# Performance work log

Hardware: AMD Instinct MI355X
Metric: run time of the kernel (lower is better)

Reference implementation:

```python
import jax, jax.numpy as jnp
import numpy as np

N_NODES = 100000
N_EDGES = 1600000
N_GRAPHS = 64
IN_DIM = 256
OUT_DIM = 512
H1 = OUT_DIM // 4   # 128
H2 = OUT_DIM // 2   # 256


def glorot(key, shape):
    lim = float(np.sqrt(6.0 / (shape[0] + shape[1])))
    return jax.random.uniform(key, shape, jnp.float32, -lim, lim)


def setup_inputs() -> dict:
    key = jax.random.key(0)
    ks = jax.random.split(key, 8)
    x = jax.random.normal(ks[0], (N_NODES, IN_DIM), jnp.float32)
    edge_index = jax.random.randint(ks[1], (2, N_EDGES), 0, N_NODES, jnp.int64)
    batch = jnp.sort(jax.random.randint(ks[2], (N_NODES,), 0, N_GRAPHS, jnp.int64))
    return {
        'x': x,
        'edge_index': edge_index,
        'batch': batch,
        'W1': glorot(ks[3], (IN_DIM, H1)),
        'b1': jnp.zeros((H1,), jnp.float32),
        'W2': glorot(ks[4], (H1, H2)),
        'b2': jnp.zeros((H2,), jnp.float32),
        'fc_W': glorot(ks[5], (H2, OUT_DIM)),
        'fc_b': jnp.zeros((OUT_DIM,), jnp.float32),
    }


def gcn_conv(x, W, b, src, dst, n_nodes):
    # PyG GCNConv (default): add self-loops, sym-normalized aggregation of XW + bias
    h = x @ W                                   # [N, F_out] transform first (cheaper gather)
    ones = jnp.ones((src.shape[0],), h.dtype)
    deg = jax.ops.segment_sum(ones, dst, num_segments=n_nodes)  # includes self-loops
    dinv = jax.lax.rsqrt(jnp.maximum(deg, 1.0))
    norm = dinv[src] * dinv[dst]                # [E]
    msg = h[src] * norm[:, None]                # gather + scale
    out = jax.ops.segment_sum(msg, dst, num_segments=n_nodes)   # scatter-add
    return out + b


def reference(x, edge_index, batch, W1, b1, W2, b2, fc_W, fc_b):
    n = x.shape[0]
    loops = jnp.arange(n, dtype=edge_index.dtype)
    src = jnp.concatenate([edge_index[0], loops])
    dst = jnp.concatenate([edge_index[1], loops])

    h = jax.nn.relu(gcn_conv(x, W1, b1, src, dst, n))   # dropout = identity (eval)
    h = jax.nn.relu(gcn_conv(h, W2, b2, src, dst, n))

    # global_mean_pool over batch ids
    sums = jax.ops.segment_sum(h, batch, num_segments=N_GRAPHS)
    cnts = jax.ops.segment_sum(jnp.ones((n,), h.dtype), batch, num_segments=N_GRAPHS)
    pooled = sums / jnp.maximum(cnts, 1.0)[:, None]     # [B, H2]

    return jax.nn.relu(pooled @ fc_W + fc_b)            # [B, OUT_DIM]
```

## Files before the change

### kernel.cpp

```cpp
#include <hip/hip_runtime.h>
#include <hip/hip_bf16.h>
#include <cstdint>

#define N_NODES 100000
#define N_EDGES 1600000
#define N_GRAPHS 64
#define IN_DIM 256
#define HD1 128
#define HD2 256
#define OUT_DIM 512

#define NBUCK 196
#define NBLK  196
#define EPB   8192

typedef __bf16 bf16x8 __attribute__((ext_vector_type(8)));
typedef float f32x4 __attribute__((ext_vector_type(4)));

static __device__ __forceinline__ float bflo(uint32_t v) { return __uint_as_float(v << 16); }
static __device__ __forceinline__ float bfhi(uint32_t v) { return __uint_as_float(v & 0xffff0000u); }
static __device__ __forceinline__ uint32_t f2bf_bits(float f) {
    uint32_t u = __float_as_uint(f);
    return (u + 0x7fffu + ((u >> 16) & 1u)) >> 16;
}
static __device__ __forceinline__ uint32_t packbf(float a, float b) {
    return f2bf_bits(a) | (f2bf_bits(b) << 16);
}
static __device__ __forceinline__ float bf2f(uint16_t b) { return __uint_as_float(((uint32_t)b) << 16); }

static __device__ __forceinline__ void gl_lds16(const void* g, void* l) {
    __builtin_amdgcn_global_load_lds((const __attribute__((address_space(1))) uint32_t*)g,
                                     (__attribute__((address_space(3))) uint32_t*)l, 16, 0, 0);
}

__global__ void k_probe(const uint32_t* __restrict__ xw, const int* __restrict__ ei,
                        int* __restrict__ flags) {
    if (threadIdx.x != 0 || blockIdx.x != 0) return;
    int mid = 0;
    for (int i = 0; i < 64; i++) {
        uint32_t f = (xw[i] >> 23) & 0xFF;
        if (f >= 64 && f < 200) mid++;
    }
    flags[0] = (mid < 32) ? 1 : 0;
    int nz = 0;
    for (int i = 0; i < 64; i++) if (ei[2 * i + 1] != 0) nz++;
    flags[1] = (nz == 0) ? 1 : 0;
}

static __device__ __forceinline__ int ld_idx(const int* p, int i, int sh) { return p[i << sh]; }
static __device__ __forceinline__ float ld_f(const void* p, int i, int isbf) {
    return isbf ? bf2f(((const uint16_t*)p)[i]) : ((const float*)p)[i];
}

__global__ __launch_bounds__(256) void k_prep(const void* __restrict__ W1, const void* __restrict__ W2,
                                              const void* __restrict__ fcW, const void* __restrict__ b1,
                                              const void* __restrict__ b2, const void* __restrict__ fcb,
                                              uint16_t* __restrict__ W1F, uint16_t* __restrict__ W2F,
                                              uint16_t* __restrict__ fcWc, uint16_t* __restrict__ bc1,
                                              uint16_t* __restrict__ bc2, uint16_t* __restrict__ fcbc,
                                              const int* __restrict__ flags) {
    int i = blockIdx.x * 256 + threadIdx.x;
    int isbf = flags[0];
    if (i < 32768) {
        int j = i & 7, l = (i >> 3) & 63, nt = (i >> 9) & 1, ks = (i >> 10) & 7, n0g = (i >> 13) & 3;
        int k = ks * 32 + (l >> 4) * 8 + j;
        int n = n0g * 32 + nt * 16 + (l & 15);
        W1F[i] = (uint16_t)f2bf_bits(ld_f(W1, k * HD1 + n, isbf));
    } else if (i < 65536) {
        int j2 = i - 32768;
        int j = j2 & 7, l = (j2 >> 3) & 63, nt = (j2 >> 9) & 1, ks = (j2 >> 10) & 3, n0g = (j2 >> 12) & 7;
        int k = ks * 32 + (l >> 4) * 8 + j;
        int n = n0g * 32 + nt * 16 + (l & 15);
        W2F[j2] = (uint16_t)f2bf_bits(ld_f(W2, k * HD2 + n, isbf));
    } else if (i < 196608) {
        int j = i - 65536;
        fcWc[j] = (uint16_t)f2bf_bits(ld_f(fcW, j, isbf));
    } else if (i < 196736) {
        bc1[i - 196608] = (uint16_t)f2bf_bits(ld_f(b1, i - 196608, isbf));
    } else if (i < 196992) {
        bc2[i - 196736] = (uint16_t)f2bf_bits(ld_f(b2, i - 196736, isbf));
    } else if (i < 197504) {
        fcbc[i - 196992] = (uint16_t)f2bf_bits(ld_f(fcb, i - 196992, isbf));
    }
}


__global__ __launch_bounds__(256) void k_hist(const int* __restrict__ ei, int* __restrict__ bh,
                                              const int* __restrict__ flags) {
    __shared__ int h[NBUCK];
    int t = threadIdx.x, blk = blockIdx.x;
    if (t < NBUCK) h[t] = 0;
    __syncthreads();
    int sh = flags[1];
    int base = blk * EPB;
#pragma unroll
    for (int k = 0; k < EPB / 256; k++) {
        int e = base + k * 256 + t;
        if (e < N_EDGES) atomicAdd(&h[ld_idx(ei, N_EDGES + e, sh) >> 9], 1);
    }
    __syncthreads();
    if (t < NBUCK) bh[blk * NBUCK + t] = h[t];
}

__global__ __launch_bounds__(256) void k_colscan(const int* __restrict__ bh, int* __restrict__ bhoff,
                                                 int* __restrict__ bucket_cnt) {
    __shared__ int s[256];
    int b = blockIdx.x, t = threadIdx.x;
    int v = (t < NBLK) ? bh[t * NBUCK + b] : 0;
    s[t] = v; __syncthreads();
    for (int off = 1; off < 256; off <<= 1) {
        int x = (t >= off) ? s[t - off] : 0;
        __syncthreads();
        s[t] += x;
        __syncthreads();
    }
    if (t < NBLK) bhoff[t * NBUCK + b] = s[t] - v;
    if (t == 255) bucket_cnt[b] = s[255];
}

__global__ __launch_bounds__(256) void k_bscan(const int* __restrict__ bucket_cnt,
                                               int* __restrict__ bucket_base,
                                               int* __restrict__ row_ptr) {
    __shared__ int s[256];
    int t = threadIdx.x;
    int v = (t < NBUCK) ? bucket_cnt[t] : 0;
    s[t] = v; __syncthreads();
    for (int off = 1; off < 256; off <<= 1) {
        int x = (t >= off) ? s[t - off] : 0;
        __syncthreads();
        s[t] += x;
        __syncthreads();
    }
    if (t < NBUCK) bucket_base[t] = s[t] - v;
    if (t == NBUCK - 1) { bucket_base[NBUCK] = s[t]; row_ptr[N_NODES] = s[t]; }
}

__global__ __launch_bounds__(256) void k_part(const int* __restrict__ ei,
                                              const int* __restrict__ bucket_base,
                                              const int* __restrict__ bhoff,
                                              int* __restrict__ tmp,
                                              const int* __restrict__ flags) {
    __shared__ int cur[NBUCK];
    int t = threadIdx.x, blk = blockIdx.x;
    if (t < NBUCK) cur[t] = bucket_base[t] + bhoff[blk * NBUCK + t];
    __syncthreads();
    int sh = flags[1];
    int base = blk * EPB;
#pragma unroll
    for (int k = 0; k < EPB / 256; k++) {
        int e = base + k * 256 + t;
        if (e < N_EDGES) {
            int s = ld_idx(ei, e, sh), d = ld_idx(ei, N_EDGES + e, sh);
            int pos = atomicAdd(&cur[d >> 9], 1);
            tmp[pos] = (s << 9) | (d & 511);
        }
    }
}

__global__ __launch_bounds__(256) void k_bsort(const int* __restrict__ tmp,
                                               const int* __restrict__ bucket_base,
                                               int* __restrict__ csr_src,
                                               int* __restrict__ row_ptr,
                                               float* __restrict__ dinv) {
    __shared__ int h[512], a[512], c[512];
    int b = blockIdx.x, t = threadIdx.x;
    int beg = bucket_base[b], end = bucket_base[b + 1];
    h[t] = 0; h[t + 256] = 0;
    __syncthreads();
    for (int i = beg + t; i < end; i += 256) atomicAdd(&h[tmp[i] & 511], 1);
    __syncthreads();
    a[t] = h[t]; a[t + 256] = h[t + 256];
    __syncthreads();
    for (int off = 1; off < 512; off <<= 1) {
        int x0 = (t >= off) ? a[t - off] : 0;
        int x1 = ((t + 256) >= off) ? a[t + 256 - off] : 0;
        __syncthreads();
        a[t] += x0; a[t + 256] += x1;
        __syncthreads();
    }
#pragma unroll
    for (int u = 0; u < 2; u++) {
        int i = t + u * 256;
        int node = (b << 9) + i;
        int ex = a[i] - h[i];
        if (node < N_NODES) {
            row_ptr[node] = beg + ex;
            dinv[node] = rsqrtf((float)(h[i] + 1));
        }
        c[i] = ex;
    }
    __syncthreads();
    for (int i = beg + t; i < end; i += 256) {
        int e = tmp[i];
        int pos = atomicAdd(&c[e & 511], 1);
        csr_src[beg + pos] = e >> 9;
    }
}

__global__ __launch_bounds__(256) void k_wpack(const int* __restrict__ csr_src,
                                               const float* __restrict__ dinv,
                                               int2* __restrict__ csr_sw) {
    int e = blockIdx.x * 256 + threadIdx.x;
    if (e < N_EDGES) {
        int s = csr_src[e];
        csr_sw[e] = make_int2(s, __float_as_int(dinv[s]));
    }
}

#define GCNT_CHUNK 8
__global__ __launch_bounds__(256) void k_gcnt(const int* __restrict__ bat, int* __restrict__ gcnt,
                                              const int* __restrict__ flags) {
    __shared__ int h[N_GRAPHS];
    int t = threadIdx.x;
    if (t < N_GRAPHS) h[t] = 0;
    __syncthreads();
    int sh = flags[1];
    int base = (blockIdx.x * 256 + t) * GCNT_CHUNK;
    int cur = -1, run = 0;
#pragma unroll
    for (int u = 0; u < GCNT_CHUNK; u++) {
        int i = base + u;
        if (i < N_NODES) {
            int g = ld_idx(bat, i, sh);
            if (g == cur) run++;
            else { if (run) atomicAdd(&h[cur], run); cur = g; run = 1; }
        }
    }
    if (run) atomicAdd(&h[cur], run);
    __syncthreads();
    if (t < N_GRAPHS) { int v = h[t]; if (v) atomicAdd(&gcnt[t], v); }
}


__global__ __launch_bounds__(256) void k_gemm1(const void* __restrict__ Ain,
                                               const uint16_t* __restrict__ BF,
                                               uint16_t* __restrict__ C,
                                               const int* __restrict__ flags) {
    __shared__ __align__(16) uint16_t As[64 * 256];
    const int M = N_NODES, N = HD1;
    int isbf = flags[0];
    int t = threadIdx.x;
    int wave = t >> 6, lane = t & 63;
    int quad = lane >> 4, l16 = lane & 15;
    int m0 = blockIdx.x * 64;
    int n0 = wave * 32;

    bf16x8 Bf[8][2];
#pragma unroll
    for (int ks = 0; ks < 8; ks++)
#pragma unroll
        for (int nt = 0; nt < 2; nt++)
            Bf[ks][nt] = *(const bf16x8*)(BF + ((((wave * 8 + ks) * 2 + nt) << 6) + lane) * 8);

    if (isbf) {
        const uint8_t* Xb = (const uint8_t*)Ain;
#pragma unroll
        for (int i = 0; i < 8; i++) {
            int o = (i * 256 + t) * 16;
            int r = o >> 9, c = o & 511;
            int rg = m0 + r; if (rg >= M) rg = M - 1;
            gl_lds16(Xb + (size_t)rg * 512 + (c ^ ((r & 7) << 4)), (uint8_t*)As + o);
        }
    } else {
        const float* Xf = (const float*)Ain;
#pragma unroll
        for (int i = 0; i < 8; i++) {
            int o = (i * 256 + t) * 16;
            int r = o >> 9, c = (o & 511) ^ ((r & 7) << 4);
            int rg = m0 + r; if (rg >= M) rg = M - 1;
            const float* p = Xf + (size_t)rg * 256 + (c >> 1);
            f32x4 f0 = *(const f32x4*)p, f1 = *(const f32x4*)(p + 4);
            union { uint16_t u[8]; bf16x8 v; } rr;
#pragma unroll
            for (int j = 0; j < 4; j++) {
                rr.u[j]     = (uint16_t)f2bf_bits(f0[j]);
                rr.u[4 + j] = (uint16_t)f2bf_bits(f1[j]);
            }
            *(bf16x8*)((uint8_t*)As + o) = rr.v;
        }
    }
    __syncthreads();

    f32x4 acc[4][2];
#pragma unroll
    for (int a = 0; a < 4; a++)
#pragma unroll
        for (int b = 0; b < 2; b++) acc[a][b] = f32x4{0.f, 0.f, 0.f, 0.f};

#pragma unroll
    for (int ks = 0; ks < 8; ks++) {
        bf16x8 af[4];
#pragma unroll
        for (int mt = 0; mt < 4; mt++) {
            int r = mt * 16 + l16;
            int cb = (ks * 64 + quad * 16) ^ ((r & 7) << 4);
            af[mt] = *(const bf16x8*)((const uint8_t*)As + r * 512 + cb);
        }
#pragma unroll
        for (int mt = 0; mt < 4; mt++)
#pragma unroll
            for (int nt = 0; nt < 2; nt++)
                acc[mt][nt] = __builtin_amdgcn_mfma_f32_16x16x32_bf16(af[mt], Bf[ks][nt], acc[mt][nt], 0, 0, 0);
    }

#pragma unroll
    for (int mt = 0; mt < 4; mt++)
#pragma unroll
        for (int reg = 0; reg < 4; reg++) {
            int row = m0 + mt * 16 + quad * 4 + reg;
            if (row < M)
#pragma unroll
                for (int nt = 0; nt < 2; nt++)
                    C[row * N + n0 + nt * 16 + l16] = (uint16_t)f2bf_bits(acc[mt][nt][reg]);
        }
}


template <int WITH_BIAS_RELU>
__global__ __launch_bounds__(256) void k_agg(const uint16_t* __restrict__ Yin, uint16_t* __restrict__ Yout,
                                             const int* __restrict__ row_ptr, const int2* __restrict__ csr_sw,
                                             const float* __restrict__ dinv, const uint16_t* __restrict__ bias) {
    int l = threadIdx.x & 63;
    int wid = (blockIdx.x << 2) | (threadIdx.x >> 6);
    const uint32_t* Y32 = (const uint32_t*)Yin;
    float b0 = 0.f, b1 = 0.f;
    if (WITH_BIAS_RELU) { b0 = bf2f(bias[2 * l]); b1 = bf2f(bias[2 * l + 1]); }
    int nbeg = __builtin_amdgcn_readfirstlane(wid * 4);

#pragma unroll 1
    for (int node = nbeg; node < nbeg + 4; node++) {
        int e0 = __builtin_amdgcn_readfirstlane(row_ptr[node]);
        int e1 = __builtin_amdgcn_readfirstlane(row_ptr[node + 1]);
        float wd = dinv[node];
        uint32_t v = Y32[(size_t)node * 64 + l];
        float a0 = wd * bflo(v), a1 = wd * bfhi(v);

        for (int e = e0; e < e1; e += 8) {
            uint32_t vv[8];
            float    ww[8];
#pragma unroll
            for (int t = 0; t < 8; t++) {
                int idx = (e + t < e1) ? e + t : e1 - 1;
                int2 sw = csr_sw[idx];
                int   s = __builtin_amdgcn_readfirstlane(sw.x);
                float w = __uint_as_float((uint32_t)__builtin_amdgcn_readfirstlane(sw.y));
                ww[t] = (e + t < e1) ? w : 0.f;
                vv[t] = Y32[(size_t)s * 64 + l];
            }
#pragma unroll
            for (int t = 0; t < 8; t++) {
                a0 += ww[t] * bflo(vv[t]);
                a1 += ww[t] * bfhi(vv[t]);
            }
        }

        a0 *= wd; a1 *= wd;
        if (WITH_BIAS_RELU) {
            a0 = fmaxf(a0 + b0, 0.f);
            a1 = fmaxf(a1 + b1, 0.f);
        }
        ((uint32_t*)Yout)[(size_t)node * 64 + l] = packbf(a0, a1);
    }
}


__global__ __launch_bounds__(512) void k_gemm2_pool(const uint16_t* __restrict__ A,
                                                    const uint16_t* __restrict__ BF,
                                                    const uint16_t* __restrict__ bias,
                                                    const int* __restrict__ bat,
                                                    const int* __restrict__ flags,
                                                    float* __restrict__ pooled) {
    __shared__ __align__(16) uint16_t As[64 * 128];
    const int M = N_NODES;
    int t = threadIdx.x;
    int wave = t >> 6, lane = t & 63;
    int quad = lane >> 4, l16 = lane & 15;
    int m0 = blockIdx.x * 64;
    int n0 = wave * 32;

    bf16x8 Bf[4][2];
#pragma unroll
    for (int ks = 0; ks < 4; ks++)
#pragma unroll
        for (int nt = 0; nt < 2; nt++)
            Bf[ks][nt] = *(const bf16x8*)(BF + ((((wave * 4 + ks) * 2 + nt) << 6) + lane) * 8);

#pragma unroll
    for (int i = 0; i < 2; i++) {
        int o = (i * 512 + t) * 16;
        int r = o >> 8, c = o & 255;
        int rg = m0 + r; if (rg >= M) rg = M - 1;
        gl_lds16((const uint8_t*)A + (size_t)rg * 256 + (c ^ ((r & 7) << 4)), (uint8_t*)As + o);
    }
    __syncthreads();

    f32x4 acc[4][2];
#pragma unroll
    for (int a = 0; a < 4; a++)
#pragma unroll
        for (int b = 0; b < 2; b++) acc[a][b] = f32x4{0.f, 0.f, 0.f, 0.f};

#pragma unroll
    for (int ks = 0; ks < 4; ks++) {
        bf16x8 af[4];
#pragma unroll
        for (int mt = 0; mt < 4; mt++) {
            int r = mt * 16 + l16;
            int cb = (ks * 64 + quad * 16) ^ ((r & 7) << 4);
            af[mt] = *(const bf16x8*)((const uint8_t*)As + r * 256 + cb);
        }
#pragma unroll
        for (int mt = 0; mt < 4; mt++)
#pragma unroll
            for (int nt = 0; nt < 2; nt++)
                acc[mt][nt] = __builtin_amdgcn_mfma_f32_16x16x32_bf16(af[mt], Bf[ks][nt], acc[mt][nt], 0, 0, 0);
    }

    int sh = flags[1];
    float bv[2];
#pragma unroll
    for (int nt = 0; nt < 2; nt++) bv[nt] = bf2f(bias[n0 + nt * 16 + l16]);

    int last = m0 + 63 < M ? m0 + 63 : M - 1;
    int gfirst = ld_idx(bat, m0, sh);
    int glast  = ld_idx(bat, last, sh);
    if ((m0 + 63 < M) && gfirst == glast) {
#pragma unroll
        for (int nt = 0; nt < 2; nt++) {
            float s = 0.f;
#pragma unroll
            for (int mt = 0; mt < 4; mt++)
#pragma unroll
                for (int reg = 0; reg < 4; reg++)
                    s += fmaxf(acc[mt][nt][reg] + bv[nt], 0.f);
            s += __shfl_xor(s, 16);
            s += __shfl_xor(s, 32);
            if (quad == 0)
                atomicAdd(&pooled[gfirst * HD2 + n0 + nt * 16 + l16], s);
        }
    } else {
#pragma unroll
        for (int mt = 0; mt < 4; mt++) {
#pragma unroll
            for (int reg = 0; reg < 4; reg++) {
                int row = m0 + mt * 16 + quad * 4 + reg;
                if (row < M) {
                    int g = ld_idx(bat, row, sh);
#pragma unroll
                    for (int nt = 0; nt < 2; nt++)
                        atomicAdd(&pooled[g * HD2 + n0 + nt * 16 + l16],
                                  fmaxf(acc[mt][nt][reg] + bv[nt], 0.f));
                }
            }
        }
    }
}


__global__ __launch_bounds__(512) void k_final(const float* __restrict__ pooled, const int* __restrict__ gcnt,
                                               const uint16_t* __restrict__ fcWc, const uint16_t* __restrict__ fcbc,
                                               void* __restrict__ out, const int* __restrict__ flags) {
    __shared__ float pm[HD2];
    int g = blockIdx.x, t = threadIdx.x;
    if (t < HD2) pm[t] = pooled[g * HD2 + t] / fmaxf((float)gcnt[g], 1.0f);
    __syncthreads();
    float acc = bf2f(fcbc[t]);
    for (int k = 0; k < HD2; k++) acc = fmaf(pm[k], bf2f(fcWc[k * OUT_DIM + t]), acc);
    acc = fmaxf(acc, 0.f);
    if (flags[0]) ((uint16_t*)out)[g * OUT_DIM + t] = (uint16_t)f2bf_bits(acc);
    else          ((float*)out)[g * OUT_DIM + t] = acc;
}


extern "C" void kernel_launch(void* const* d_in, const int* in_sizes, int n_in,
                              void* d_out, int out_size, void* d_ws, size_t ws_size,
                              hipStream_t stream) {
    const void* x   = d_in[0];
    const int*  ei  = (const int*)d_in[1];
    const int*  bat = (const int*)d_in[2];
    const void* W1  = d_in[3];
    const void* b1  = d_in[4];
    const void* W2  = d_in[5];
    const void* b2  = d_in[6];
    const void* fcW = d_in[7];
    const void* fcb = d_in[8];

    char* ws = (char*)d_ws;
    size_t off = 0;
    auto alloc = [&](size_t bytes) -> void* {
        void* p = ws + off;
        off += (bytes + 255) & ~(size_t)255;
        return p;
    };
    uint16_t* buf0 = (uint16_t*)alloc((size_t)N_NODES * HD1 * 2);
    uint16_t* Hb   = (uint16_t*)alloc((size_t)N_NODES * HD1 * 2);
    int*   row_ptr = (int*)alloc((N_NODES + 1) * 4);
    int*   csr_src = (int*)alloc((size_t)N_EDGES * 4);
    int2*  csr_sw  = (int2*)alloc((size_t)N_EDGES * 8);
    int*   tmp     = (int*)alloc((size_t)N_EDGES * 4);
    int*   bh      = (int*)alloc(NBLK * NBUCK * 4);
    int*   bhoff   = (int*)alloc(NBLK * NBUCK * 4);
    int*   bucket_cnt  = (int*)alloc(NBUCK * 4);
    int*   bucket_base = (int*)alloc((NBUCK + 1) * 4);
    float* dinv    = (float*)alloc(N_NODES * 4);
    int*   gcnt    = (int*)alloc(N_GRAPHS * 4);
    float* pooled  = (float*)alloc(N_GRAPHS * HD2 * 4);
    uint16_t* W1T  = (uint16_t*)alloc(IN_DIM * HD1 * 2);
    uint16_t* W2T  = (uint16_t*)alloc(HD1 * HD2 * 2);
    uint16_t* bc1  = (uint16_t*)alloc(HD1 * 2);
    uint16_t* bc2  = (uint16_t*)alloc(HD2 * 2);
    uint16_t* fcWc = (uint16_t*)alloc(HD2 * OUT_DIM * 2);
    uint16_t* fcbc = (uint16_t*)alloc(OUT_DIM * 2);
    int*   flags   = (int*)alloc(64 * 4);

    uint16_t* Y1 = buf0;
    uint16_t* Zb = buf0;

    hipMemsetAsync(gcnt, 0, N_GRAPHS * 4, stream);
    hipMemsetAsync(pooled, 0, N_GRAPHS * HD2 * 4, stream);

    k_probe<<<1, 64, 0, stream>>>((const uint32_t*)x, ei, flags);

    k_prep<<<(197504 + 255) / 256, 256, 0, stream>>>(W1, W2, fcW, b1, b2, fcb,
                                                     W1T, W2T, fcWc, bc1, bc2, fcbc, flags);

    k_hist<<<NBLK, 256, 0, stream>>>(ei, bh, flags);
    k_colscan<<<NBUCK, 256, 0, stream>>>(bh, bhoff, bucket_cnt);
    k_bscan<<<1, 256, 0, stream>>>(bucket_cnt, bucket_base, row_ptr);
    k_part<<<NBLK, 256, 0, stream>>>(ei, bucket_base, bhoff, tmp, flags);
    k_bsort<<<NBUCK, 256, 0, stream>>>(tmp, bucket_base, csr_src, row_ptr, dinv);
    k_wpack<<<N_EDGES / 256, 256, 0, stream>>>(csr_src, dinv, csr_sw);

    k_gcnt<<<(N_NODES + 256 * GCNT_CHUNK - 1) / (256 * GCNT_CHUNK), 256, 0, stream>>>(bat, gcnt, flags);

    k_gemm1<<<(N_NODES + 63) / 64, 256, 0, stream>>>(x, W1T, Y1, flags);
    k_agg<1><<<N_NODES / 16, 256, 0, stream>>>(Y1, Hb, row_ptr, csr_sw, dinv, bc1);

    k_agg<0><<<N_NODES / 16, 256, 0, stream>>>(Hb, Zb, row_ptr, csr_sw, dinv, nullptr);
    k_gemm2_pool<<<(N_NODES + 63) / 64, 512, 0, stream>>>(Zb, W2T, bc2, bat, flags, pooled);

    k_final<<<N_GRAPHS, 512, 0, stream>>>(pooled, gcnt, fcWc, fcbc, d_out, flags);
}
```

Measured before the change: 438.7 us.

## Restructure SpMM aggregation: one node per wave, four edges per 16-lane group

```diff
diff --git a/kernel.cpp b/kernel.cpp
--- a/kernel.cpp
+++ b/kernel.cpp
@@ -16,6 +16,7 @@
 
 typedef __bf16 bf16x8 __attribute__((ext_vector_type(8)));
 typedef float f32x4 __attribute__((ext_vector_type(4)));
+typedef uint32_t u32x4 __attribute__((ext_vector_type(4)));
 
 static __device__ __forceinline__ float bflo(uint32_t v) { return __uint_as_float(v << 16); }
 static __device__ __forceinline__ float bfhi(uint32_t v) { return __uint_as_float(v & 0xffff0000u); }
@@ -320,46 +321,77 @@
 __global__ __launch_bounds__(256) void k_agg(const uint16_t* __restrict__ Yin, uint16_t* __restrict__ Yout,
                                              const int* __restrict__ row_ptr, const int2* __restrict__ csr_sw,
                                              const float* __restrict__ dinv, const uint16_t* __restrict__ bias) {
+    int node = blockIdx.x * 4 + (threadIdx.x >> 6);
     int l = threadIdx.x & 63;
-    int wid = (blockIdx.x << 2) | (threadIdx.x >> 6);
-    const uint32_t* Y32 = (const uint32_t*)Yin;
-    float b0 = 0.f, b1 = 0.f;
-    if (WITH_BIAS_RELU) { b0 = bf2f(bias[2 * l]); b1 = bf2f(bias[2 * l + 1]); }
-    int nbeg = __builtin_amdgcn_readfirstlane(wid * 4);
-
-#pragma unroll 1
-    for (int node = nbeg; node < nbeg + 4; node++) {
-        int e0 = __builtin_amdgcn_readfirstlane(row_ptr[node]);
-        int e1 = __builtin_amdgcn_readfirstlane(row_ptr[node + 1]);
-        float wd = dinv[node];
-        uint32_t v = Y32[(size_t)node * 64 + l];
-        float a0 = wd * bflo(v), a1 = wd * bfhi(v);
-
-        for (int e = e0; e < e1; e += 8) {
-            uint32_t vv[8];
-            float    ww[8];
-#pragma unroll
-            for (int t = 0; t < 8; t++) {
-                int idx = (e + t < e1) ? e + t : e1 - 1;
-                int2 sw = csr_sw[idx];
-                int   s = __builtin_amdgcn_readfirstlane(sw.x);
-                float w = __uint_as_float((uint32_t)__builtin_amdgcn_readfirstlane(sw.y));
-                ww[t] = (e + t < e1) ? w : 0.f;
-                vv[t] = Y32[(size_t)s * 64 + l];
+    int grp = l >> 4;
+    int c16 = l & 15;
+    const u32x4* Y4 = (const u32x4*)Yin;
+
+    float wd = dinv[node];
+    float a[8];
+    {
+        u32x4 v = Y4[(size_t)node * 16 + c16];
+        float w = (grp == 0) ? wd : 0.f;
+#pragma unroll
+        for (int j = 0; j < 4; j++) {
+            a[2 * j]     = w * bflo(v[j]);
+            a[2 * j + 1] = w * bfhi(v[j]);
+        }
+    }
+
+    int e0 = row_ptr[node], e1 = row_ptr[node + 1];
+    for (int cb = e0; cb < e1; cb += 64) {
+        int cnt = e1 - cb; if (cnt > 64) cnt = 64;
+        int my_s = 0, my_w = 0;
+        if (l < cnt) { int2 sw = csr_sw[cb + l]; my_s = sw.x; my_w = sw.y; }
+        int mrounds = (cnt + 15) >> 4;
+        for (int r = 0; r < mrounds; r++) {
+            u32x4 vv[4];
+            float ww[4];
+#pragma unroll
+            for (int q = 0; q < 4; q++) {
+                int base = r * 16 + q * 4;
+                int s0 = __builtin_amdgcn_readlane(my_s, base + 0);
+                int s1 = __builtin_amdgcn_readlane(my_s, base + 1);
+                int s2 = __builtin_amdgcn_readlane(my_s, base + 2);
+                int s3 = __builtin_amdgcn_readlane(my_s, base + 3);
+                int w0 = __builtin_amdgcn_readlane(my_w, base + 0);
+                int w1 = __builtin_amdgcn_readlane(my_w, base + 1);
+                int w2 = __builtin_amdgcn_readlane(my_w, base + 2);
+                int w3 = __builtin_amdgcn_readlane(my_w, base + 3);
+                int s = (grp == 0) ? s0 : (grp == 1) ? s1 : (grp == 2) ? s2 : s3;
+                int w = (grp == 0) ? w0 : (grp == 1) ? w1 : (grp == 2) ? w2 : w3;
+                ww[q] = __uint_as_float((uint32_t)w);
+                vv[q] = Y4[(size_t)s * 16 + c16];
             }
 #pragma unroll
-            for (int t = 0; t < 8; t++) {
-                a0 += ww[t] * bflo(vv[t]);
-                a1 += ww[t] * bfhi(vv[t]);
+            for (int q = 0; q < 4; q++)
+#pragma unroll
+                for (int j = 0; j < 4; j++) {
+                    a[2 * j]     += ww[q] * bflo(vv[q][j]);
+                    a[2 * j + 1] += ww[q] * bfhi(vv[q][j]);
+                }
+        }
+    }
+
+#pragma unroll
+    for (int j = 0; j < 8; j++) {
+        a[j] += __shfl_xor(a[j], 16);
+        a[j] += __shfl_xor(a[j], 32);
+    }
+
+    if (grp == 0) {
+        uint32_t o[4];
+#pragma unroll
+        for (int j = 0; j < 4; j++) {
+            float x0 = a[2 * j] * wd, x1 = a[2 * j + 1] * wd;
+            if (WITH_BIAS_RELU) {
+                x0 = fmaxf(x0 + bf2f(bias[c16 * 8 + 2 * j]), 0.f);
+                x1 = fmaxf(x1 + bf2f(bias[c16 * 8 + 2 * j + 1]), 0.f);
             }
-        }
-
-        a0 *= wd; a1 *= wd;
-        if (WITH_BIAS_RELU) {
-            a0 = fmaxf(a0 + b0, 0.f);
-            a1 = fmaxf(a1 + b1, 0.f);
-        }
-        ((uint32_t*)Yout)[(size_t)node * 64 + l] = packbf(a0, a1);
+            o[j] = packbf(x0, x1);
+        }
+        *(u32x4*)((uint32_t*)Yout + (size_t)node * 64 + c16 * 4) = u32x4{o[0], o[1], o[2], o[3]};
     }
 }
 
@@ -534,9 +566,9 @@
     k_gcnt<<<(N_NODES + 256 * GCNT_CHUNK - 1) / (256 * GCNT_CHUNK), 256, 0, stream>>>(bat, gcnt, flags);
 
     k_gemm1<<<(N_NODES + 63) / 64, 256, 0, stream>>>(x, W1T, Y1, flags);
-    k_agg<1><<<N_NODES / 16, 256, 0, stream>>>(Y1, Hb, row_ptr, csr_sw, dinv, bc1);
-
-    k_agg<0><<<N_NODES / 16, 256, 0, stream>>>(Hb, Zb, row_ptr, csr_sw, dinv, nullptr);
+    k_agg<1><<<N_NODES / 4, 256, 0, stream>>>(Y1, Hb, row_ptr, csr_sw, dinv, bc1);
+
+    k_agg<0><<<N_NODES / 4, 256, 0, stream>>>(Hb, Zb, row_ptr, csr_sw, dinv, nullptr);
     k_gemm2_pool<<<(N_NODES + 63) / 64, 512, 0, stream>>>(Zb, W2T, bc2, bat, flags, pooled);
 
     k_final<<<N_GRAPHS, 512, 0, stream>>>(pooled, gcnt, fcWc, fcbc, d_out, flags);
```

After: 438.9 us. Within noise of the previous version (+0.0%).
